# Performance work log

Measured on AMD Instinct MI355X. Metric: run time of the kernel, lower is better.

Reference implementation:

```python
import jax, jax.numpy as jnp
import numpy as np

D_MODEL = 1024
N_HEAD = 16
D_K = 64
D_V = 64
LN_EPS = 1e-5


def setup_inputs() -> dict:
    key = jax.random.key(0)
    ks = jax.random.split(key, 12)
    B, S = 4, 2048
    s = 1.0 / np.sqrt(D_MODEL)
    inp = {
        "q": jax.random.normal(ks[0], (B, S, D_MODEL), jnp.float32),
        "k": jax.random.normal(ks[1], (B, S, D_MODEL), jnp.float32),
        "v": jax.random.normal(ks[2], (B, S, D_MODEL), jnp.float32),
        "mask": jnp.ones((B, S, S), jnp.int32),
        "w_q": jax.random.normal(ks[3], (D_MODEL, N_HEAD * D_K), jnp.float32) * s,
        "b_q": jnp.zeros((N_HEAD * D_K,), jnp.float32),
        "w_k": jax.random.normal(ks[4], (D_MODEL, N_HEAD * D_K), jnp.float32) * s,
        "b_k": jnp.zeros((N_HEAD * D_K,), jnp.float32),
        "w_v": jax.random.normal(ks[5], (D_MODEL, N_HEAD * D_V), jnp.float32) * s,
        "b_v": jnp.zeros((N_HEAD * D_V,), jnp.float32),
        "w_fc": jax.random.normal(ks[6], (N_HEAD * D_V, D_MODEL), jnp.float32) * s,
        "b_fc": jnp.zeros((D_MODEL,), jnp.float32),
        "ln_g": jnp.ones((D_MODEL,), jnp.float32),
        "ln_b": jnp.zeros((D_MODEL,), jnp.float32),
    }
    return inp


def reference(q, k, v, mask, w_q, b_q, w_k, b_k, w_v, b_v, w_fc, b_fc, ln_g, ln_b):
    B, Sq, _ = q.shape
    Sk = k.shape[1]
    residual = q
    # QKV projections -> [B, H, S, d]
    qh = (q @ w_q + b_q).reshape(B, Sq, N_HEAD, D_K).transpose(0, 2, 1, 3)
    kh = (k @ w_k + b_k).reshape(B, Sk, N_HEAD, D_K).transpose(0, 2, 1, 3)
    vh = (v @ w_v + b_v).reshape(B, Sk, N_HEAD, D_V).transpose(0, 2, 1, 3)
    temp = jnp.sqrt(jnp.asarray(D_K, qh.dtype))
    scores = jnp.einsum("bhqd,bhkd->bhqk", qh / temp, kh)
    scores = jnp.where(mask[:, None, :, :] == 0, jnp.asarray(-1e9, scores.dtype), scores)
    attn = jax.nn.softmax(scores, axis=-1)  # dropout is identity in eval
    out = jnp.einsum("bhqk,bhkd->bhqd", attn, vh)
    out = out.transpose(0, 2, 1, 3).reshape(B, Sq, N_HEAD * D_V)
    out = out @ w_fc + b_fc  # output proj (dropout identity)
    x = out + residual
    mu = jnp.mean(x, axis=-1, keepdims=True)
    var = jnp.mean(jnp.square(x - mu), axis=-1, keepdims=True)
    y = (x - mu) * jax.lax.rsqrt(var + LN_EPS) * ln_g + ln_b
    return (y, attn)
```

## Files before the change

kernel.cpp:

```cpp
#include <hip/hip_runtime.h>
#include <cstdint>
#include <cstddef>

#define DM 1024
#define HN 16
#define DH 64
#define BB 4
#define SS 2048
#define MM (BB * SS)

typedef __bf16 bf16;
typedef bf16 bf16x8 __attribute__((ext_vector_type(8)));
typedef bf16 bf16x4 __attribute__((ext_vector_type(4)));
typedef float f32x4 __attribute__((ext_vector_type(4)));

__device__ __forceinline__ f32x4 mfma16(bf16x8 a, bf16x8 b, f32x4 c) {
  return __builtin_amdgcn_mfma_f32_16x16x32_bf16(a, b, c, 0, 0, 0);
}

typedef __attribute__((address_space(3))) void lds_void_t;
typedef __attribute__((address_space(1))) void glob_void_t;

__device__ __forceinline__ void gload16(const void* g, void* l) {
  __builtin_amdgcn_global_load_lds((const glob_void_t*)g, (lds_void_t*)l, 16, 0, 0);
}

__global__ __launch_bounds__(256) void mask_bits(const int* __restrict__ mask,
                                                 unsigned long long* __restrict__ mbits) {
  size_t i = (size_t)blockIdx.x * 256 + threadIdx.x;
  int m = mask[i];
  unsigned long long w = __ballot(m != 0);
  if ((threadIdx.x & 63) == 0) mbits[i >> 6] = w;
}

__global__ __launch_bounds__(256) void cvt3(const float* __restrict__ q,
                                            const float* __restrict__ k,
                                            const float* __restrict__ v,
                                            bf16* __restrict__ dst) {
  int which = blockIdx.y;
  const float* in = which == 0 ? q : which == 1 ? k : v;
  bf16* out = dst + (size_t)which * MM * DM;
  int i = (blockIdx.x * 256 + threadIdx.x) * 8;
  f32x4 a = *(const f32x4*)(in + i);
  f32x4 b = *(const f32x4*)(in + i + 4);
  bf16x8 o;
  o[0] = (bf16)a[0]; o[1] = (bf16)a[1]; o[2] = (bf16)a[2]; o[3] = (bf16)a[3];
  o[4] = (bf16)b[0]; o[5] = (bf16)b[1]; o[6] = (bf16)b[2]; o[7] = (bf16)b[3];
  *(bf16x8*)(out + i) = o;
}

__global__ __launch_bounds__(256) void wtrans4(const float* __restrict__ w_q,
                                               const float* __restrict__ w_k,
                                               const float* __restrict__ w_v,
                                               const float* __restrict__ w_fc,
                                               bf16* __restrict__ WT) {
  int p = blockIdx.z;
  const float* W = p == 0 ? w_q : p == 1 ? w_k : p == 2 ? w_v : w_fc;
  bf16* out = WT + (size_t)p * DM * DM;
  __shared__ float t[32][33];
  int n0 = blockIdx.x * 32, k0 = blockIdx.y * 32;
  int tid = threadIdx.x;
  int r = tid >> 3, c = (tid & 7) * 4;
  f32x4 v = *(const f32x4*)&W[(size_t)(k0 + r) * DM + n0 + c];
  t[r][c] = v[0]; t[r][c + 1] = v[1]; t[r][c + 2] = v[2]; t[r][c + 3] = v[3];
  __syncthreads();
  bf16x4 o;
#pragma unroll
  for (int i = 0; i < 4; ++i) o[i] = (bf16)t[c + i][r];
  *(bf16x4*)&out[(size_t)(n0 + r) * DM + k0 + c] = o;
}

__global__ __launch_bounds__(256) void gemm_qkv(const bf16* __restrict__ Abase,
                                                const bf16* __restrict__ Bt,
                                                const float* __restrict__ b_q,
                                                const float* __restrict__ b_k,
                                                const float* __restrict__ b_v,
                                                bf16* __restrict__ qhh,
                                                bf16* __restrict__ khh,
                                                bf16* __restrict__ vhT) {
  constexpr int K = DM;
  __shared__ bf16 Ab[128 * 32];
  __shared__ bf16 Bb[128 * 32];
  int tid = threadIdx.x, wave = tid >> 6, lane = tid & 63;
  int bm = blockIdx.x * 128, bn = blockIdx.y * 128;
  int proj = bn >> 10;
  const bf16* A = Abase + (size_t)proj * MM * DM;
  const float* bias = proj == 0 ? b_q : proj == 1 ? b_k : b_v;
  int wr = (wave >> 1) * 64, wc = (wave & 1) * 64;
  int fr = lane & 15, kg8 = (lane >> 4) * 8;
  f32x4 acc[4][4] = {};
  int arow = tid >> 2, acol = (tid & 3) * 8;
  const bf16* Ag0 = A + (size_t)(bm + arow) * K + acol;
  const bf16* Ag1 = Ag0 + (size_t)64 * K;
  const bf16* Bg0 = Bt + (size_t)(bn + arow) * K + acol;
  const bf16* Bg1 = Bg0 + (size_t)64 * K;
  char* la = (char*)Ab + wave * 1024;
  char* lb = (char*)Bb + wave * 1024;
  for (int k0 = 0; k0 < K; k0 += 32) {
    __syncthreads();
    gload16(Ag0 + k0, la);
    gload16(Ag1 + k0, la + 4096);
    gload16(Bg0 + k0, lb);
    gload16(Bg1 + k0, lb + 4096);
    asm volatile("s_waitcnt vmcnt(0)" ::: "memory");
    __syncthreads();
    bf16x8 af[4], bfr[4];
#pragma unroll
    for (int m = 0; m < 4; ++m)
      af[m] = *(const bf16x8*)&Ab[(wr + m * 16 + fr) * 32 + kg8];
#pragma unroll
    for (int n = 0; n < 4; ++n)
      bfr[n] = *(const bf16x8*)&Bb[(wc + n * 16 + fr) * 32 + kg8];
#pragma unroll
    for (int m = 0; m < 4; ++m)
#pragma unroll
      for (int n = 0; n < 4; ++n) acc[m][n] = mfma16(af[m], bfr[n], acc[m][n]);
  }
  int b = bm >> 11;
#pragma unroll
  for (int m = 0; m < 4; ++m)
#pragma unroll
    for (int n = 0; n < 4; ++n) {
      int c = bn + wc + n * 16 + fr;
      int lc = c & 1023;
      float bv = bias[lc];
      int h = lc >> 6, d = lc & 63;
      int r0 = bm + wr + m * 16 + (lane >> 4) * 4;
      int s0 = r0 & (SS - 1);
      if (proj == 2) {
        bf16x4 o;
#pragma unroll
        for (int j = 0; j < 4; ++j) o[j] = (bf16)(acc[m][n][j] + bv);
        *(bf16x4*)&vhT[(size_t)(b * HN + h) * (SS * DH) +
                       (size_t)(s0 >> 5) * (DH * 32) + d * 32 + (s0 & 31)] = o;
      } else {
        bf16* dst = proj == 0 ? qhh : khh;
        float sc = proj == 0 ? 0.125f : 1.f;
#pragma unroll
        for (int j = 0; j < 4; ++j) {
          float v = (acc[m][n][j] + bv) * sc;
          dst[(size_t)(b * HN + h) * (SS * DH) + (size_t)(s0 + j) * DH + d] =
              (bf16)v;
        }
      }
    }
}

__global__ __launch_bounds__(256) void gemm_out(const bf16* __restrict__ A,
                                                const bf16* __restrict__ Bt,
                                                const float* __restrict__ bias,
                                                const float* __restrict__ resid,
                                                float* __restrict__ out) {
  constexpr int K = DM;
  __shared__ bf16 Ab[128 * 32];
  __shared__ bf16 Bb[128 * 32];
  int tid = threadIdx.x, wave = tid >> 6, lane = tid & 63;
  int bm = blockIdx.x * 128, bn = blockIdx.y * 128;
  int wr = (wave >> 1) * 64, wc = (wave & 1) * 64;
  int fr = lane & 15, kg8 = (lane >> 4) * 8;
  f32x4 acc[4][4] = {};
  int arow = tid >> 2, acol = (tid & 3) * 8;
  const bf16* Ag0 = A + (size_t)(bm + arow) * K + acol;
  const bf16* Ag1 = Ag0 + (size_t)64 * K;
  const bf16* Bg0 = Bt + (size_t)(bn + arow) * K + acol;
  const bf16* Bg1 = Bg0 + (size_t)64 * K;
  char* la = (char*)Ab + wave * 1024;
  char* lb = (char*)Bb + wave * 1024;
  for (int k0 = 0; k0 < K; k0 += 32) {
    __syncthreads();
    gload16(Ag0 + k0, la);
    gload16(Ag1 + k0, la + 4096);
    gload16(Bg0 + k0, lb);
    gload16(Bg1 + k0, lb + 4096);
    asm volatile("s_waitcnt vmcnt(0)" ::: "memory");
    __syncthreads();
    bf16x8 af[4], bfr[4];
#pragma unroll
    for (int m = 0; m < 4; ++m)
      af[m] = *(const bf16x8*)&Ab[(wr + m * 16 + fr) * 32 + kg8];
#pragma unroll
    for (int n = 0; n < 4; ++n)
      bfr[n] = *(const bf16x8*)&Bb[(wc + n * 16 + fr) * 32 + kg8];
#pragma unroll
    for (int m = 0; m < 4; ++m)
#pragma unroll
      for (int n = 0; n < 4; ++n) acc[m][n] = mfma16(af[m], bfr[n], acc[m][n]);
  }
#pragma unroll
  for (int m = 0; m < 4; ++m)
#pragma unroll
    for (int n = 0; n < 4; ++n) {
      int c = bn + wc + n * 16 + fr;
      float bv = bias[c];
#pragma unroll
      for (int j = 0; j < 4; ++j) {
        int r = bm + wr + m * 16 + (lane >> 4) * 4 + j;
        size_t idx = (size_t)r * DM + c;
        out[idx] = acc[m][n][j] + bv + resid[idx];
      }
    }
}

__global__ __launch_bounds__(512, 4) void attn_kernel(
    const bf16* __restrict__ qh, const bf16* __restrict__ kh,
    const bf16* __restrict__ vhT, const unsigned int* __restrict__ mbits,
    float* __restrict__ attn_out, bf16* __restrict__ ctx) {
  extern __shared__ char smem[];
  float* pbuf = (float*)(smem + 16 * 4096);
  float* invp = (float*)(smem + 16 * 4096 + 4096);
  int tid = threadIdx.x, wave = tid >> 6, lane = tid & 63;
  int qt = blockIdx.x, bh = blockIdx.y;
  int b = bh >> 4, h = bh & 15;
  int q0 = qt * 16;
  const bf16* qbase = qh + ((size_t)bh * SS + q0) * DH;
  const bf16* kbase = kh + (size_t)bh * SS * DH;
  const bf16* vbase = vhT + (size_t)bh * SS * DH;
  int fr = lane & 15, kg = lane >> 4;

  bf16x8 qf0 = *(const bf16x8*)&qbase[(size_t)fr * DH + kg * 8];
  bf16x8 qf1 = *(const bf16x8*)&qbase[(size_t)fr * DH + 32 + kg * 8];

  {
    int sw = wave * 256;
    bf16x8 kb0[8], kb1[8];
    auto kload = [&](int g) {
      const bf16* kp = kbase + (size_t)(sw + g * 16 + fr) * DH + kg * 8;
      kb0[g & 7] = *(const bf16x8*)kp;
      kb1[g & 7] = *(const bf16x8*)(kp + 32);
    };
#pragma unroll
    for (int g = 0; g < 6; ++g) kload(g);
#pragma unroll
    for (int g = 0; g < 16; ++g) {
      if (g < 10) kload(g + 6);
      f32x4 acc = {0.f, 0.f, 0.f, 0.f};
      acc = mfma16(qf0, kb0[g & 7], acc);
      acc = mfma16(qf1, kb1[g & 7], acc);
      int col = sw + g * 16 + fr;
      int slot = col >> 3, within = col & 7;
#pragma unroll
      for (int j = 0; j < 4; ++j) {
        int row = kg * 4 + j;
        *(bf16*)(smem + row * 4096 + ((slot ^ row) << 4) + within * 2) =
            (bf16)acc[j];
      }
    }
  }
  __syncthreads();

  {
    int row = wave * 2 + (lane >> 5);
    int la = lane & 31;
    char* rbase = smem + row * 4096;
    const unsigned int* mrow32 = mbits + ((size_t)b * SS + q0 + row) * 64;
    float sum = 0.f;
#pragma unroll
    for (int it = 0; it < 8; ++it) {
      int slot = la + it * 32;
      char* p = rbase + ((slot ^ row) << 4);
      bf16x8 e = *(const bf16x8*)p;
      unsigned int bits = mrow32[slot >> 2] >> ((slot & 3) * 8);
      bf16x8 w8;
#pragma unroll
      for (int i = 0; i < 8; ++i) {
        float f = __expf((float)e[i]);
        f = ((bits >> i) & 1u) ? f : 0.f;
        sum += f;
        w8[i] = (bf16)f;
      }
      *(bf16x8*)p = w8;
    }
#pragma unroll
    for (int off = 1; off < 32; off <<= 1) sum += __shfl_xor(sum, off);
    if (la == 0) invp[row] = 1.f / sum;
  }
  __syncthreads();

  {
    int slot = tid >> 1;
    int halfoff = (tid & 1) * 8;
    float* outbase = attn_out + ((size_t)bh * SS + q0) * SS + tid * 4;
#pragma unroll
    for (int r = 0; r < 16; ++r) {
      bf16x4 e = *(const bf16x4*)(smem + r * 4096 + ((slot ^ r) << 4) + halfoff);
      float inv = invp[r];
      f32x4 u = {(float)e[0] * inv, (float)e[1] * inv, (float)e[2] * inv,
                 (float)e[3] * inv};
      *(f32x4*)(outbase + (size_t)r * SS) = u;
    }
  }

  {
    int dq = wave & 3, khalf = wave >> 2;
    f32x4 cacc = {0.f, 0.f, 0.f, 0.f};
    const bf16* vtile = vbase + (size_t)(khalf * 32) * (DH * 32) +
                        (dq * 16 + fr) * 32 + kg * 8;
    char* prow = smem + fr * 4096;
    bf16x8 vb[8], pb[8];
    auto pvload = [&](int kk) {
      vb[kk & 7] = *(const bf16x8*)&vtile[(size_t)kk * (DH * 32)];
      int slotA = khalf * 128 + kk * 4 + kg;
      pb[kk & 7] = *(const bf16x8*)(prow + ((slotA ^ fr) << 4));
    };
    pvload(0);
    pvload(1);
    pvload(2);
    pvload(3);
#pragma unroll
    for (int kk = 0; kk < 32; ++kk) {
      if (kk < 28) pvload(kk + 4);
      cacc = mfma16(pb[kk & 7], vb[kk & 7], cacc);
    }
    if (khalf == 1) {
#pragma unroll
      for (int j = 0; j < 4; ++j)
        pbuf[dq * 256 + (kg * 4 + j) * 16 + fr] = cacc[j];
    }
    __syncthreads();
    if (khalf == 0) {
#pragma unroll
      for (int j = 0; j < 4; ++j) {
        int row = kg * 4 + j;
        float v = (cacc[j] + pbuf[dq * 256 + row * 16 + fr]) * invp[row];
        ctx[((size_t)b * SS + q0 + row) * DM + h * DH + dq * 16 + fr] = (bf16)v;
      }
    }
  }
}

__global__ __launch_bounds__(256) void ln_k(float* __restrict__ x,
                                            const float* __restrict__ g,
                                            const float* __restrict__ bln) {
  int r = blockIdx.x, tid = threadIdx.x;
  f32x4 v = *(const f32x4*)&x[(size_t)r * DM + tid * 4];
  float s = v[0] + v[1] + v[2] + v[3];
  float s2 = v[0] * v[0] + v[1] * v[1] + v[2] * v[2] + v[3] * v[3];
#pragma unroll
  for (int off = 32; off; off >>= 1) {
    s += __shfl_down(s, off);
    s2 += __shfl_down(s2, off);
  }
  __shared__ float rs_[4], rs2_[4];
  int wave = tid >> 6, lane = tid & 63;
  if (lane == 0) {
    rs_[wave] = s;
    rs2_[wave] = s2;
  }
  __syncthreads();
  s = rs_[0] + rs_[1] + rs_[2] + rs_[3];
  s2 = rs2_[0] + rs2_[1] + rs2_[2] + rs2_[3];
  float mu = s * (1.f / DM);
  float var = s2 * (1.f / DM) - mu * mu;
  float rstd = rsqrtf(var + 1e-5f);
  f32x4 gg = *(const f32x4*)&g[tid * 4];
  f32x4 bb = *(const f32x4*)&bln[tid * 4];
  f32x4 o;
#pragma unroll
  for (int i = 0; i < 4; ++i) o[i] = (v[i] - mu) * rstd * gg[i] + bb[i];
  *(f32x4*)&x[(size_t)r * DM + tid * 4] = o;
}

extern "C" void kernel_launch(void* const* d_in, const int* in_sizes, int n_in,
                              void* d_out, int out_size, void* d_ws,
                              size_t ws_size, hipStream_t stream) {
  const float* q = (const float*)d_in[0];
  const float* k = (const float*)d_in[1];
  const float* v = (const float*)d_in[2];
  const int* mask = (const int*)d_in[3];
  const float* w_q = (const float*)d_in[4];
  const float* b_q = (const float*)d_in[5];
  const float* w_k = (const float*)d_in[6];
  const float* b_k = (const float*)d_in[7];
  const float* w_v = (const float*)d_in[8];
  const float* b_v = (const float*)d_in[9];
  const float* w_fc = (const float*)d_in[10];
  const float* b_fc = (const float*)d_in[11];
  const float* ln_g = (const float*)d_in[12];
  const float* ln_b = (const float*)d_in[13];

  float* y = (float*)d_out;
  float* attn_out = (float*)d_out + (size_t)MM * DM;

  char* w = (char*)d_ws;
  const size_t actN = (size_t)MM * DM;
  bf16* qkv_bf = (bf16*)w;  w += 3 * actN * 2;
  bf16* wT = (bf16*)w;      w += (size_t)4 * DM * DM * 2;
  bf16* qhh = (bf16*)w;     w += actN * 2;
  bf16* khh = (bf16*)w;     w += actN * 2;
  bf16* vhT = (bf16*)w;     w += actN * 2;
  bf16* ctx = (bf16*)w;     w += actN * 2;
  unsigned long long* mb = (unsigned long long*)w;  w += (size_t)BB * SS * SS / 8;

  mask_bits<<<(BB * SS * SS) / 256, 256, 0, stream>>>(mask, mb);
  cvt3<<<dim3(4096, 3), 256, 0, stream>>>(q, k, v, qkv_bf);
  wtrans4<<<dim3(DM / 32, DM / 32, 4), 256, 0, stream>>>(w_q, w_k, w_v, w_fc, wT);
  gemm_qkv<<<dim3(MM / 128, 3072 / 128), 256, 0, stream>>>(
      qkv_bf, wT, b_q, b_k, b_v, qhh, khh, vhT);
  hipFuncSetAttribute((const void*)attn_kernel,
                      hipFuncAttributeMaxDynamicSharedMemorySize, 69696);
  attn_kernel<<<dim3(SS / 16, BB * HN), 512, 69696, stream>>>(
      qhh, khh, vhT, (const unsigned int*)mb, attn_out, ctx);
  gemm_out<<<dim3(MM / 128, DM / 128), 256, 0, stream>>>(
      ctx, wT + (size_t)3 * DM * DM, b_fc, q, y);
  ln_k<<<MM, 256, 0, stream>>>(y, ln_g, ln_b);
}
```

Before: 731.5 us.

## Double attention query tile to 32 rows and remap blocks across XCDs

Each attention block now handles 32 query rows with 1024 threads instead of 16 rows with 512 threads. Every loaded K fragment feeds two MFMA chains, which halves K traffic per query row. The launch becomes 1D with a block index remap that keeps each (batch, head)'s query tiles on the same XCD, so their shared K/V stay in the same L2. LDS use doubles to about 136 KB per block, which limits each CU to one block; the number of resident waves per CU stays roughly the same, but there are fewer blocks to hide latency and tail effects.

```diff
diff --git a/kernel.cpp b/kernel.cpp
--- a/kernel.cpp
+++ b/kernel.cpp
@@ -201,27 +201,30 @@
     }
 }
 
-__global__ __launch_bounds__(512, 4) void attn_kernel(
+__global__ __launch_bounds__(1024, 4) void attn_kernel(
     const bf16* __restrict__ qh, const bf16* __restrict__ kh,
     const bf16* __restrict__ vhT, const unsigned int* __restrict__ mbits,
     float* __restrict__ attn_out, bf16* __restrict__ ctx) {
   extern __shared__ char smem[];
-  float* pbuf = (float*)(smem + 16 * 4096);
-  float* invp = (float*)(smem + 16 * 4096 + 4096);
+  float* pbuf = (float*)(smem + 32 * 4096);
+  float* invp = (float*)(smem + 32 * 4096 + 8192);
   int tid = threadIdx.x, wave = tid >> 6, lane = tid & 63;
-  int qt = blockIdx.x, bh = blockIdx.y;
+  int fid = (blockIdx.x & 7) * 512 + (blockIdx.x >> 3);
+  int bh = fid >> 6, qt = fid & 63;
   int b = bh >> 4, h = bh & 15;
-  int q0 = qt * 16;
+  int q0 = qt * 32;
   const bf16* qbase = qh + ((size_t)bh * SS + q0) * DH;
   const bf16* kbase = kh + (size_t)bh * SS * DH;
   const bf16* vbase = vhT + (size_t)bh * SS * DH;
   int fr = lane & 15, kg = lane >> 4;
 
-  bf16x8 qf0 = *(const bf16x8*)&qbase[(size_t)fr * DH + kg * 8];
-  bf16x8 qf1 = *(const bf16x8*)&qbase[(size_t)fr * DH + 32 + kg * 8];
+  bf16x8 qa0 = *(const bf16x8*)&qbase[(size_t)fr * DH + kg * 8];
+  bf16x8 qa1 = *(const bf16x8*)&qbase[(size_t)fr * DH + 32 + kg * 8];
+  bf16x8 qb0 = *(const bf16x8*)&qbase[(size_t)(16 + fr) * DH + kg * 8];
+  bf16x8 qb1 = *(const bf16x8*)&qbase[(size_t)(16 + fr) * DH + 32 + kg * 8];
 
   {
-    int sw = wave * 256;
+    int sw = wave * 128;
     bf16x8 kb0[8], kb1[8];
     auto kload = [&](int g) {
       const bf16* kp = kbase + (size_t)(sw + g * 16 + fr) * DH + kg * 8;
@@ -229,20 +232,26 @@
       kb1[g & 7] = *(const bf16x8*)(kp + 32);
     };
 #pragma unroll
-    for (int g = 0; g < 6; ++g) kload(g);
-#pragma unroll
-    for (int g = 0; g < 16; ++g) {
-      if (g < 10) kload(g + 6);
-      f32x4 acc = {0.f, 0.f, 0.f, 0.f};
-      acc = mfma16(qf0, kb0[g & 7], acc);
-      acc = mfma16(qf1, kb1[g & 7], acc);
+    for (int g = 0; g < 4; ++g) kload(g);
+#pragma unroll
+    for (int g = 0; g < 8; ++g) {
+      if (g < 4) kload(g + 4);
+      f32x4 aa = {0.f, 0.f, 0.f, 0.f};
+      f32x4 ab = {0.f, 0.f, 0.f, 0.f};
+      aa = mfma16(qa0, kb0[g & 7], aa);
+      aa = mfma16(qa1, kb1[g & 7], aa);
+      ab = mfma16(qb0, kb0[g & 7], ab);
+      ab = mfma16(qb1, kb1[g & 7], ab);
       int col = sw + g * 16 + fr;
       int slot = col >> 3, within = col & 7;
 #pragma unroll
       for (int j = 0; j < 4; ++j) {
-        int row = kg * 4 + j;
-        *(bf16*)(smem + row * 4096 + ((slot ^ row) << 4) + within * 2) =
-            (bf16)acc[j];
+        int ra = kg * 4 + j;
+        int rb = ra + 16;
+        *(bf16*)(smem + ra * 4096 + ((slot ^ ra) << 4) + within * 2) =
+            (bf16)aa[j];
+        *(bf16*)(smem + rb * 4096 + ((slot ^ rb) << 4) + within * 2) =
+            (bf16)ab[j];
       }
     }
   }
@@ -277,30 +286,32 @@
   __syncthreads();
 
   {
-    int slot = tid >> 1;
-    int halfoff = (tid & 1) * 8;
-    float* outbase = attn_out + ((size_t)bh * SS + q0) * SS + tid * 4;
-#pragma unroll
-    for (int r = 0; r < 16; ++r) {
+    int t = tid & 511, rh = tid >> 9;
+    int slot = t >> 1, halfoff = (t & 1) * 8;
+    float* outb = attn_out + ((size_t)bh * SS + q0) * SS;
+#pragma unroll
+    for (int it = 0; it < 16; ++it) {
+      int r = it * 2 + rh;
       bf16x4 e = *(const bf16x4*)(smem + r * 4096 + ((slot ^ r) << 4) + halfoff);
       float inv = invp[r];
       f32x4 u = {(float)e[0] * inv, (float)e[1] * inv, (float)e[2] * inv,
                  (float)e[3] * inv};
-      *(f32x4*)(outbase + (size_t)r * SS) = u;
+      *(f32x4*)(outb + (size_t)r * SS + t * 4) = u;
     }
   }
 
   {
-    int dq = wave & 3, khalf = wave >> 2;
+    int rb = wave >> 3, dq = (wave >> 1) & 3, kh2 = wave & 1;
     f32x4 cacc = {0.f, 0.f, 0.f, 0.f};
-    const bf16* vtile = vbase + (size_t)(khalf * 32) * (DH * 32) +
+    const bf16* vtile = vbase + (size_t)(kh2 * 32) * (DH * 32) +
                         (dq * 16 + fr) * 32 + kg * 8;
-    char* prow = smem + fr * 4096;
+    int prow_row = rb * 16 + fr;
+    char* prow = smem + prow_row * 4096;
     bf16x8 vb[8], pb[8];
     auto pvload = [&](int kk) {
       vb[kk & 7] = *(const bf16x8*)&vtile[(size_t)kk * (DH * 32)];
-      int slotA = khalf * 128 + kk * 4 + kg;
-      pb[kk & 7] = *(const bf16x8*)(prow + ((slotA ^ fr) << 4));
+      int slotA = kh2 * 128 + kk * 4 + kg;
+      pb[kk & 7] = *(const bf16x8*)(prow + ((slotA ^ prow_row) << 4));
     };
     pvload(0);
     pvload(1);
@@ -311,17 +322,18 @@
       if (kk < 28) pvload(kk + 4);
       cacc = mfma16(pb[kk & 7], vb[kk & 7], cacc);
     }
-    if (khalf == 1) {
+    if (kh2 == 1) {
 #pragma unroll
       for (int j = 0; j < 4; ++j)
-        pbuf[dq * 256 + (kg * 4 + j) * 16 + fr] = cacc[j];
+        pbuf[((rb * 4 + dq) * 16 + kg * 4 + j) * 16 + fr] = cacc[j];
     }
     __syncthreads();
-    if (khalf == 0) {
+    if (kh2 == 0) {
 #pragma unroll
       for (int j = 0; j < 4; ++j) {
-        int row = kg * 4 + j;
-        float v = (cacc[j] + pbuf[dq * 256 + row * 16 + fr]) * invp[row];
+        int row = rb * 16 + kg * 4 + j;
+        float v = (cacc[j] + pbuf[((rb * 4 + dq) * 16 + kg * 4 + j) * 16 + fr]) *
+                  invp[row];
         ctx[((size_t)b * SS + q0 + row) * DM + h * DH + dq * 16 + fr] = (bf16)v;
       }
     }
@@ -397,8 +409,8 @@
   gemm_qkv<<<dim3(MM / 128, 3072 / 128), 256, 0, stream>>>(
       qkv_bf, wT, b_q, b_k, b_v, qhh, khh, vhT);
   hipFuncSetAttribute((const void*)attn_kernel,
-                      hipFuncAttributeMaxDynamicSharedMemorySize, 69696);
-  attn_kernel<<<dim3(SS / 16, BB * HN), 512, 69696, stream>>>(
+                      hipFuncAttributeMaxDynamicSharedMemorySize, 139392);
+  attn_kernel<<<4096, 1024, 139392, stream>>>(
       qhh, khh, vhT, (const unsigned int*)mb, attn_out, ctx);
   gemm_out<<<dim3(MM / 128, DM / 128), 256, 0, stream>>>(
       ctx, wT + (size_t)3 * DM * DM, b_fc, q, y);
```

After: 671.1 us. -8.3%, faster.
